# Optimization experiments

Measured on AMD Instinct MI355X. Metric: run time of the kernel, lower is better.

Reference implementation:

```python
import jax, jax.numpy as jnp
import numpy as np

PARENTS = np.array([-1, 0, 1, 1, 1])
NECK_CHAIN = np.array([1, 0])  # neck joint (1) up to root (0)
B, V, F, J, S, E = 512, 5023, 9976, 5, 100, 50
L_STAT, L_DYN, L_FULL, N_BUCKET = 51, 17, 68, 79


def rodrigues(rvec):
    """Axis-angle [N,3] -> rotation matrices [N,3,3]."""
    angle = jnp.linalg.norm(rvec + 1e-8, axis=-1, keepdims=True)  # [N,1]
    axis = rvec / angle
    s = jnp.sin(angle)[..., None]
    c = jnp.cos(angle)[..., None]
    rx, ry, rz = axis[:, 0], axis[:, 1], axis[:, 2]
    z = jnp.zeros_like(rx)
    K = jnp.stack([z, -rz, ry, rz, z, -rx, -ry, rx, z], axis=-1).reshape(-1, 3, 3)
    I = jnp.eye(3, dtype=rvec.dtype)
    return I + s * K + (1.0 - c) * (K @ K)


def verts2lmk(vertices, faces, lmk_faces_idx, lmk_bary):
    lmk_faces = faces[lmk_faces_idx]                               # [B,L,3]
    lmk_verts = jax.vmap(lambda v, f: v[f])(vertices, lmk_faces)   # [B,L,3verts,3xyz]
    return jnp.einsum('blfc,blf->blc', lmk_verts, lmk_bary)


def setup_inputs() -> dict:
    key = jax.random.key(0)
    ks = jax.random.split(key, 16)
    shape_params = jax.random.normal(ks[0], (B, S), jnp.float32)
    expression_params = jax.random.normal(ks[1], (B, E), jnp.float32)
    pose_params = 0.2 * jax.random.normal(ks[2], (B, 6), jnp.float32)
    eye_pose_params = 0.1 * jax.random.normal(ks[3], (B, 6), jnp.float32)
    v_template = jax.random.normal(ks[4], (V, 3), jnp.float32) * 0.1
    shapedirs = jax.random.normal(ks[5], (V, 3, S + E), jnp.float32) * 0.01
    posedirs = jax.random.normal(ks[6], ((J - 1) * 9, V * 3), jnp.float32) * 0.01
    jr = jax.random.uniform(ks[7], (J, V), jnp.float32)
    J_regressor = jr / jnp.sum(jr, axis=1, keepdims=True)
    lbs_weights = jax.nn.softmax(jax.random.normal(ks[8], (V, J), jnp.float32), axis=-1)
    faces = jax.random.randint(ks[9], (F, 3), 0, V)
    lmk_faces_idx = jax.random.randint(ks[10], (L_STAT,), 0, F)
    lb = jax.random.uniform(ks[11], (L_STAT, 3), jnp.float32) + 1e-3
    lmk_bary_coords = lb / jnp.sum(lb, axis=-1, keepdims=True)
    dynamic_lmk_faces_idx = jax.random.randint(ks[12], (N_BUCKET, L_DYN), 0, F)
    db = jax.random.uniform(ks[13], (N_BUCKET, L_DYN, 3), jnp.float32) + 1e-3
    dynamic_lmk_bary_coords = db / jnp.sum(db, axis=-1, keepdims=True)
    full_lmk_faces_idx = jax.random.randint(ks[14], (L_FULL,), 0, F)
    fb = jax.random.uniform(ks[15], (L_FULL, 3), jnp.float32) + 1e-3
    full_lmk_bary_coords = fb / jnp.sum(fb, axis=-1, keepdims=True)
    return {
        'shape_params': shape_params, 'expression_params': expression_params,
        'pose_params': pose_params, 'eye_pose_params': eye_pose_params,
        'v_template': v_template, 'shapedirs': shapedirs, 'posedirs': posedirs,
        'J_regressor': J_regressor, 'lbs_weights': lbs_weights, 'faces': faces,
        'lmk_faces_idx': lmk_faces_idx, 'lmk_bary_coords': lmk_bary_coords,
        'dynamic_lmk_faces_idx': dynamic_lmk_faces_idx,
        'dynamic_lmk_bary_coords': dynamic_lmk_bary_coords,
        'full_lmk_faces_idx': full_lmk_faces_idx,
        'full_lmk_bary_coords': full_lmk_bary_coords,
    }


def reference(shape_params, expression_params, pose_params, eye_pose_params,
              v_template, shapedirs, posedirs, J_regressor, lbs_weights, faces,
              lmk_faces_idx, lmk_bary_coords, dynamic_lmk_faces_idx,
              dynamic_lmk_bary_coords, full_lmk_faces_idx, full_lmk_bary_coords):
    b = shape_params.shape[0]
    nv = v_template.shape[0]
    dt = shape_params.dtype
    betas = jnp.concatenate([shape_params, expression_params], axis=1)          # [B,150]
    neck = jnp.zeros((b, 3), dtype=dt)
    full_pose = jnp.concatenate(
        [pose_params[:, :3], neck, pose_params[:, 3:], eye_pose_params], axis=1)  # [B,15]
    # shape + expression blendshapes
    v_shaped = v_template[None] + jnp.einsum('bl,vcl->bvc', betas, shapedirs)   # [B,V,3]
    joints = jnp.einsum('jv,bvc->bjc', J_regressor, v_shaped)                   # [B,5,3]
    rot_mats = rodrigues(full_pose.reshape(-1, 3)).reshape(b, J, 3, 3)          # [B,5,3,3]
    I3 = jnp.eye(3, dtype=dt)
    pose_feature = (rot_mats[:, 1:] - I3).reshape(b, -1)                        # [B,36]
    v_posed = v_shaped + (pose_feature @ posedirs).reshape(b, nv, 3)
    # kinematic chain -> global joint transforms
    rel_J = joints.at[:, 1:].add(-joints[:, PARENTS[1:]])
    tm = jnp.zeros((b, J, 4, 4), dtype=dt)
    tm = tm.at[:, :, :3, :3].set(rot_mats).at[:, :, :3, 3].set(rel_J).at[:, :, 3, 3].set(1.0)
    chain = [tm[:, 0]]
    for i in range(1, J):
        chain.append(chain[PARENTS[i]] @ tm[:, i])
    A = jnp.stack(chain, axis=1)                                                # [B,5,4,4]
    Rj = jnp.einsum('bjmn,bjn->bjm', A[:, :, :3, :3], joints)
    A_rel = A.at[:, :, :3, 3].add(-Rj)
    # per-vertex skinning
    T = jnp.einsum('vj,bjmn->bvmn', lbs_weights, A_rel)                         # [B,V,4,4]
    vertices = jnp.einsum('bvmn,bvn->bvm', T[:, :, :3, :3], v_posed) + T[:, :, :3, 3]
    # dynamic contour landmark selection from neck kin-chain relative rotation
    aa = full_pose.reshape(b, J, 3)[:, NECK_CHAIN]                              # [B,2,3]
    rc = rodrigues(aa.reshape(-1, 3)).reshape(b, len(NECK_CHAIN), 3, 3)
    rel_rot = jnp.broadcast_to(I3, (b, 3, 3))
    for idx in range(len(NECK_CHAIN)):
        rel_rot = rc[:, idx] @ rel_rot
    sy = jnp.sqrt(rel_rot[:, 0, 0] ** 2 + rel_rot[:, 1, 0] ** 2)
    y_deg = jnp.arctan2(-rel_rot[:, 2, 0], sy) * (180.0 / np.pi)
    y_rot = jnp.round(jnp.minimum(y_deg, 39.0)).astype(jnp.int32)
    neg_mask = y_rot < 0
    big_neg = y_rot < -39
    neg_vals = jnp.where(big_neg, 78, 39 - y_rot)
    y_rot = jnp.where(neg_mask, neg_vals, y_rot)                                # [B] in [0,79)
    dyn_faces = dynamic_lmk_faces_idx[y_rot]                                    # [B,17]
    dyn_bary = dynamic_lmk_bary_coords[y_rot]                                   # [B,17,3]
    lf = jnp.concatenate([dyn_faces, jnp.broadcast_to(lmk_faces_idx[None], (b, lmk_faces_idx.shape[0]))], axis=1)
    lb = jnp.concatenate([dyn_bary, jnp.broadcast_to(lmk_bary_coords[None], (b,) + lmk_bary_coords.shape)], axis=1)
    landmarks2d = verts2lmk(vertices, faces, lf, lb)
    ff = jnp.broadcast_to(full_lmk_faces_idx[None], (b, full_lmk_faces_idx.shape[0]))
    fb = jnp.broadcast_to(full_lmk_bary_coords[None], (b,) + full_lmk_bary_coords.shape)
    landmarks3d = verts2lmk(vertices, faces, ff, fb)
    return (vertices, landmarks2d, landmarks3d)
```

## Files before the change

### kernel.cpp

```cpp
#include <hip/hip_runtime.h>
#include <cstddef>
#include <cstdint>

#define cB   512
#define cV   5023
#define cS   100
#define cE   50
#define cJ   5
#define cLD  17
#define cLF  68

#define cV3    15069
#define cNPAD  15072
#define cKPAD  192

#define OUT_V  ((size_t)cB * cV * 3)
#define OUT_L  ((size_t)cB * cLF * 3)

#define WS_BTN   ((size_t)0)
#define WS_ATM   (WS_BTN + (size_t)cNPAD * 96)
#define WS_JS    (WS_ATM + (size_t)cB * 96)
#define WS_AREL  (WS_JS + 2272)
#define WS_PF    (WS_AREL + (size_t)cB * 60)
#define WS_YROT  (WS_PF + (size_t)cB * 36)

typedef __attribute__((ext_vector_type(8))) short short8;
typedef __attribute__((ext_vector_type(4))) float f32x4;

__device__ __forceinline__ unsigned short f2bf(float x) {
  unsigned int u = __float_as_uint(x);
  u = (u + 0x7fffu + ((u >> 16) & 1u)) >> 16;
  return (unsigned short)u;
}

__device__ __forceinline__ void rodrigues9(float rx, float ry, float rz, float* R) {
  float a0 = rx + 1e-8f, a1 = ry + 1e-8f, a2 = rz + 1e-8f;
  float angle = sqrtf(a0 * a0 + a1 * a1 + a2 * a2);
  float inv = 1.0f / angle;
  float x = rx * inv, y = ry * inv, z = rz * inv;
  float s = sinf(angle), c = cosf(angle);
  float t = 1.0f - c;
  float xy = x * y, xz = x * z, yz = y * z;
  R[0] = 1.0f - t * (y * y + z * z);
  R[1] = -s * z + t * xy;
  R[2] =  s * y + t * xz;
  R[3] =  s * z + t * xy;
  R[4] = 1.0f - t * (x * x + z * z);
  R[5] = -s * x + t * yz;
  R[6] = -s * y + t * xz;
  R[7] =  s * x + t * yz;
  R[8] = 1.0f - t * (x * x + y * y);
}

__global__ void k_js(const float* __restrict__ jreg, const float* __restrict__ sd,
                     const float* __restrict__ vt, float* __restrict__ JS) {
  int t = threadIdx.x;
  if (t >= 453) return;
  int c = t / 151, l = t - c * 151;
  int v0 = blockIdx.x * 40;
  int v1 = v0 + 40; if (v1 > cV) v1 = cV;
  float acc[5] = {0.f, 0.f, 0.f, 0.f, 0.f};
  for (int v = v0; v < v1; ++v) {
    float x = (l < 150) ? sd[(size_t)(v * 3 + c) * 150 + l] : vt[v * 3 + c];
#pragma unroll
    for (int j = 0; j < 5; ++j)
      acc[j] = fmaf(jreg[j * cV + v], x, acc[j]);
  }
#pragma unroll
  for (int j = 0; j < 5; ++j)
    atomicAdd(&JS[(j * 3 + c) * 151 + l], acc[j]);
}

__global__ void k_batch(const float* __restrict__ shp, const float* __restrict__ expr,
                        const float* __restrict__ pose, const float* __restrict__ eyep,
                        const float* __restrict__ JSg, float* __restrict__ Arel,
                        float* __restrict__ pf, int* __restrict__ yrot) {
  __shared__ float js[2272];
  for (int i = threadIdx.x; i < 2265; i += 64) js[i] = JSg[i];
  __syncthreads();
  int b = blockIdx.x * 64 + threadIdx.x;
  if (b >= cB) return;
  float jnt[5][3];
#pragma unroll
  for (int j = 0; j < 5; ++j)
#pragma unroll
    for (int c = 0; c < 3; ++c)
      jnt[j][c] = js[(j * 3 + c) * 151 + 150];
  for (int l = 0; l < 150; ++l) {
    float beta = (l < cS) ? shp[b * cS + l] : expr[b * cE + (l - cS)];
#pragma unroll
    for (int j = 0; j < 5; ++j)
#pragma unroll
      for (int c = 0; c < 3; ++c)
        jnt[j][c] = fmaf(beta, js[(j * 3 + c) * 151 + l], jnt[j][c]);
  }
  float fp[5][3];
  fp[0][0] = pose[b * 6 + 0]; fp[0][1] = pose[b * 6 + 1]; fp[0][2] = pose[b * 6 + 2];
  fp[1][0] = 0.f; fp[1][1] = 0.f; fp[1][2] = 0.f;
  fp[2][0] = pose[b * 6 + 3]; fp[2][1] = pose[b * 6 + 4]; fp[2][2] = pose[b * 6 + 5];
  fp[3][0] = eyep[b * 6 + 0]; fp[3][1] = eyep[b * 6 + 1]; fp[3][2] = eyep[b * 6 + 2];
  fp[4][0] = eyep[b * 6 + 3]; fp[4][1] = eyep[b * 6 + 4]; fp[4][2] = eyep[b * 6 + 5];
  float R[5][9];
#pragma unroll
  for (int j = 0; j < 5; ++j) rodrigues9(fp[j][0], fp[j][1], fp[j][2], R[j]);
#pragma unroll
  for (int j = 1; j < 5; ++j)
#pragma unroll
    for (int r = 0; r < 9; ++r) {
      float id = (r == 0 || r == 4 || r == 8) ? 1.f : 0.f;
      pf[b * 36 + (j - 1) * 9 + r] = R[j][r] - id;
    }
  float rel[5][3];
#pragma unroll
  for (int c = 0; c < 3; ++c) {
    rel[0][c] = jnt[0][c];
    rel[1][c] = jnt[1][c] - jnt[0][c];
    rel[2][c] = jnt[2][c] - jnt[1][c];
    rel[3][c] = jnt[3][c] - jnt[1][c];
    rel[4][c] = jnt[4][c] - jnt[1][c];
  }
  float GR[5][9], Gt[5][3];
#pragma unroll
  for (int r = 0; r < 9; ++r) GR[0][r] = R[0][r];
#pragma unroll
  for (int c = 0; c < 3; ++c) Gt[0][c] = rel[0][c];
  const int par[5] = {0, 0, 1, 1, 1};
#pragma unroll
  for (int j = 1; j < 5; ++j) {
    int p = par[j];
#pragma unroll
    for (int r = 0; r < 3; ++r) {
#pragma unroll
      for (int cc = 0; cc < 3; ++cc)
        GR[j][r * 3 + cc] = GR[p][r * 3 + 0] * R[j][0 + cc] +
                            GR[p][r * 3 + 1] * R[j][3 + cc] +
                            GR[p][r * 3 + 2] * R[j][6 + cc];
      Gt[j][r] = Gt[p][r] + GR[p][r * 3 + 0] * rel[j][0] +
                            GR[p][r * 3 + 1] * rel[j][1] +
                            GR[p][r * 3 + 2] * rel[j][2];
    }
  }
#pragma unroll
  for (int j = 0; j < 5; ++j)
#pragma unroll
    for (int r = 0; r < 3; ++r) {
      float tj = Gt[j][r] - (GR[j][r * 3 + 0] * jnt[j][0] +
                             GR[j][r * 3 + 1] * jnt[j][1] +
                             GR[j][r * 3 + 2] * jnt[j][2]);
      Arel[b * 60 + j * 12 + r * 4 + 0] = GR[j][r * 3 + 0];
      Arel[b * 60 + j * 12 + r * 4 + 1] = GR[j][r * 3 + 1];
      Arel[b * 60 + j * 12 + r * 4 + 2] = GR[j][r * 3 + 2];
      Arel[b * 60 + j * 12 + r * 4 + 3] = tj;
    }
  float Ra[9], Rb[9];
  rodrigues9(fp[1][0], fp[1][1], fp[1][2], Ra);
  rodrigues9(fp[0][0], fp[0][1], fp[0][2], Rb);
  float r00 = Rb[0] * Ra[0] + Rb[1] * Ra[3] + Rb[2] * Ra[6];
  float r10 = Rb[3] * Ra[0] + Rb[4] * Ra[3] + Rb[5] * Ra[6];
  float r20 = Rb[6] * Ra[0] + Rb[7] * Ra[3] + Rb[8] * Ra[6];
  float sy = sqrtf(r00 * r00 + r10 * r10);
  float ydeg = atan2f(-r20, sy) * 57.29577951308232f;
  int y = (int)rintf(fminf(ydeg, 39.0f));
  if (y < 0) y = (y < -39) ? 78 : (39 - y);
  yrot[b] = y;
}

#define QB ((size_t)cNPAD * 48)
__global__ void k_prep(const float* __restrict__ sd, const float* __restrict__ shp,
                       const float* __restrict__ expr, const float* __restrict__ pfm,
                       unsigned int* __restrict__ btn_u2, unsigned int* __restrict__ atm_u2) {
  size_t idx = (size_t)blockIdx.x * 256 + threadIdx.x;
  unsigned short o[4];
  if (idx < QB) {
    int n = (int)(idx / 48), kq = (int)(idx - (size_t)n * 48);
#pragma unroll
    for (int j = 0; j < 4; ++j) {
      int k = kq * 4 + j;
      float v = (n < cV3 && k < 150) ? sd[(size_t)n * 150 + k] : 0.f;
      o[j] = f2bf(v);
    }
    btn_u2[idx * 2 + 0] = (unsigned int)o[0] | ((unsigned int)o[1] << 16);
    btn_u2[idx * 2 + 1] = (unsigned int)o[2] | ((unsigned int)o[3] << 16);
  } else {
    size_t r = idx - QB;
    int m = (int)(r / 48), kq = (int)(r - (size_t)m * 48);
#pragma unroll
    for (int j = 0; j < 4; ++j) {
      int k = kq * 4 + j;
      float v;
      if (k < cS)            v = shp[m * cS + k];
      else if (k < 150)      v = expr[m * cE + (k - cS)];
      else if (k < 186)      v = pfm[m * 36 + (k - 150)];
      else                   v = 0.f;
      o[j] = f2bf(v);
    }
    atm_u2[r * 2 + 0] = (unsigned int)o[0] | ((unsigned int)o[1] << 16);
    atm_u2[r * 2 + 1] = (unsigned int)o[2] | ((unsigned int)o[3] << 16);
  }
}

__global__ void k_pdT(const float* __restrict__ pd, unsigned int* __restrict__ btn_u) {
  __shared__ unsigned short T[64 * 36];
  const int t = threadIdx.x;
  const int n0 = blockIdx.x * 64;
#pragma unroll
  for (int it = 0; it < 9; ++it) {
    int e = t + it * 256;
    int kk = e >> 6, ln = e & 63;
    int n = n0 + ln;
    float v = (n < cV3) ? pd[(size_t)kk * cV3 + n] : 0.f;
    T[ln * 36 + kk] = f2bf(v);
  }
  __syncthreads();
  for (int e = t; e < 64 * 18; e += 256) {
    int ln = e / 18, d = e - ln * 18;
    int n = n0 + ln;
    if (n < cV3) {
      unsigned int w = (unsigned int)T[ln * 36 + 2 * d] |
                       ((unsigned int)T[ln * 36 + 2 * d + 1] << 16);
      btn_u[(size_t)n * 96 + 75 + d] = w;
    }
  }
}

__global__ __launch_bounds__(256) void k_main(
    const unsigned short* __restrict__ BTn, const unsigned short* __restrict__ ATm,
    const float* __restrict__ Arel, const float* __restrict__ vtempl,
    const float* __restrict__ lbw, float* __restrict__ out) {
  __shared__ __align__(16) unsigned short smem[32000];
  unsigned short* As = smem;
  unsigned short* Bs = smem + 12800;
  float* Pf  = (float*)smem;
  float* ArL = ((float*)smem) + 6528;

  const int t  = threadIdx.x;
  const int nb = blockIdx.x, mb = blockIdx.y;

  {
    const unsigned short* bsrc = BTn + (size_t)nb * 96 * 192;
    const unsigned short* asrc = ATm + (size_t)mb * 64 * 192;
#pragma unroll
    for (int it = 0; it < 15; ++it) {
      int e = t + it * 256;
      uint4 val;
      int row, col;
      if (e < 2304) {
        row = e / 24; col = e - row * 24;
        val = *(const uint4*)(bsrc + (size_t)e * 8);
        *(uint4*)(Bs + row * 200 + col * 8) = val;
      } else {
        int e2 = e - 2304;
        row = e2 / 24; col = e2 - row * 24;
        val = *(const uint4*)(asrc + (size_t)e2 * 8);
        *(uint4*)(As + row * 200 + col * 8) = val;
      }
    }
  }
  __syncthreads();

  const int w = t >> 6, L = t & 63;
  const int wm = w >> 1, wn = w & 1;
  const int lr = L & 15, lq = L >> 4;

  f32x4 acc[2][3];
#pragma unroll
  for (int mt = 0; mt < 2; ++mt)
#pragma unroll
    for (int nt = 0; nt < 3; ++nt) acc[mt][nt] = (f32x4){0.f, 0.f, 0.f, 0.f};

#pragma unroll
  for (int ks = 0; ks < 6; ++ks) {
    const int ko = ks * 32 + lq * 8;
    short8 af[2], bf[3];
#pragma unroll
    for (int mt = 0; mt < 2; ++mt)
      af[mt] = *(const short8*)(As + (wm * 32 + mt * 16 + lr) * 200 + ko);
#pragma unroll
    for (int nt = 0; nt < 3; ++nt)
      bf[nt] = *(const short8*)(Bs + (wn * 48 + nt * 16 + lr) * 200 + ko);
#pragma unroll
    for (int mt = 0; mt < 2; ++mt)
#pragma unroll
      for (int nt = 0; nt < 3; ++nt)
        acc[mt][nt] = __builtin_amdgcn_mfma_f32_16x16x32_bf16(af[mt], bf[nt], acc[mt][nt], 0, 0, 0);
  }
  __syncthreads();

#pragma unroll
  for (int mt = 0; mt < 2; ++mt)
#pragma unroll
    for (int nt = 0; nt < 3; ++nt) {
      int m_base = wm * 32 + mt * 16 + lq * 4;
      int n_loc  = wn * 48 + nt * 16 + lr;
      *(f32x4*)(Pf + n_loc * 68 + m_base) = acc[mt][nt];
    }
  for (int e = t; e < 3840; e += 256)
    ArL[e] = Arel[(size_t)mb * 64 * 60 + e];
  __syncthreads();

  const int v_loc = t & 31, bgrp = t >> 5;
  const int v = nb * 32 + v_loc;
  float wj[5], vtl[3];
  const bool vok = (v < cV);
#pragma unroll
  for (int j = 0; j < 5; ++j) wj[j] = vok ? lbw[v * 5 + j] : 0.f;
#pragma unroll
  for (int c = 0; c < 3; ++c) vtl[c] = vok ? vtempl[v * 3 + c] : 0.f;

#pragma unroll
  for (int i = 0; i < 8; ++i) {
    const int b_loc = bgrp * 8 + i;
    const float* q = ArL + b_loc * 60;
    float px = Pf[(v_loc * 3 + 0) * 68 + b_loc] + vtl[0];
    float py = Pf[(v_loc * 3 + 1) * 68 + b_loc] + vtl[1];
    float pz = Pf[(v_loc * 3 + 2) * 68 + b_loc] + vtl[2];
    float o0 = 0.f, o1 = 0.f, o2 = 0.f;
#pragma unroll
    for (int j = 0; j < 5; ++j) {
      f32x4 q0 = *(const f32x4*)(q + j * 12);
      f32x4 q1 = *(const f32x4*)(q + j * 12 + 4);
      f32x4 q2 = *(const f32x4*)(q + j * 12 + 8);
      float s0 = q0.x * px + q0.y * py + q0.z * pz + q0.w;
      float s1 = q1.x * px + q1.y * py + q1.z * pz + q1.w;
      float s2 = q2.x * px + q2.y * py + q2.z * pz + q2.w;
      o0 = fmaf(wj[j], s0, o0);
      o1 = fmaf(wj[j], s1, o1);
      o2 = fmaf(wj[j], s2, o2);
    }
    if (vok) {
      const int b = mb * 64 + b_loc;
      size_t off = ((size_t)b * cV + v) * 3;
      out[off + 0] = o0;
      out[off + 1] = o1;
      out[off + 2] = o2;
    }
  }
}

__global__ void k_lmk(const float* __restrict__ verts, const int* __restrict__ faces,
                      const int* __restrict__ lmkf, const float* __restrict__ lmkb,
                      const int* __restrict__ dynf, const float* __restrict__ dynb,
                      const int* __restrict__ fullf, const float* __restrict__ fullb,
                      const int* __restrict__ yrot, float* __restrict__ out) {
  int id = blockIdx.x * 256 + threadIdx.x;
  if (id >= cB * cLF) return;
  int b = id / cLF, l = id - b * cLF;
  const float* vb = verts + (size_t)b * cV * 3;
  {
    int f; float w0, w1, w2;
    if (l < cLD) {
      int yb = yrot[b];
      f = dynf[yb * cLD + l];
      const float* bp = dynb + ((size_t)yb * cLD + l) * 3;
      w0 = bp[0]; w1 = bp[1]; w2 = bp[2];
    } else {
      f = lmkf[l - cLD];
      const float* bp = lmkb + (size_t)(l - cLD) * 3;
      w0 = bp[0]; w1 = bp[1]; w2 = bp[2];
    }
    int i0 = faces[f * 3 + 0] * 3, i1 = faces[f * 3 + 1] * 3, i2 = faces[f * 3 + 2] * 3;
    size_t o = OUT_V + ((size_t)b * cLF + l) * 3;
    out[o + 0] = w0 * vb[i0 + 0] + w1 * vb[i1 + 0] + w2 * vb[i2 + 0];
    out[o + 1] = w0 * vb[i0 + 1] + w1 * vb[i1 + 1] + w2 * vb[i2 + 1];
    out[o + 2] = w0 * vb[i0 + 2] + w1 * vb[i1 + 2] + w2 * vb[i2 + 2];
  }
  {
    int f = fullf[l];
    const float* bp = fullb + (size_t)l * 3;
    float w0 = bp[0], w1 = bp[1], w2 = bp[2];
    int i0 = faces[f * 3 + 0] * 3, i1 = faces[f * 3 + 1] * 3, i2 = faces[f * 3 + 2] * 3;
    size_t o = OUT_V + OUT_L + ((size_t)b * cLF + l) * 3;
    out[o + 0] = w0 * vb[i0 + 0] + w1 * vb[i1 + 0] + w2 * vb[i2 + 0];
    out[o + 1] = w0 * vb[i0 + 1] + w1 * vb[i1 + 1] + w2 * vb[i2 + 1];
    out[o + 2] = w0 * vb[i0 + 2] + w1 * vb[i1 + 2] + w2 * vb[i2 + 2];
  }
}

extern "C" void kernel_launch(void* const* d_in, const int* in_sizes, int n_in,
                              void* d_out, int out_size, void* d_ws, size_t ws_size,
                              hipStream_t stream) {
  (void)in_sizes; (void)n_in; (void)out_size; (void)ws_size;
  const float* shp  = (const float*)d_in[0];
  const float* expr = (const float*)d_in[1];
  const float* pose = (const float*)d_in[2];
  const float* eyep = (const float*)d_in[3];
  const float* vt   = (const float*)d_in[4];
  const float* sd   = (const float*)d_in[5];
  const float* pd   = (const float*)d_in[6];
  const float* jreg = (const float*)d_in[7];
  const float* lbw  = (const float*)d_in[8];
  const int*   fcs  = (const int*)d_in[9];
  const int*   lmkf = (const int*)d_in[10];
  const float* lmkb = (const float*)d_in[11];
  const int*   dynf = (const int*)d_in[12];
  const float* dynb = (const float*)d_in[13];
  const int*   fullf= (const int*)d_in[14];
  const float* fullb= (const float*)d_in[15];
  float* out = (float*)d_out;
  float* ws  = (float*)d_ws;

  unsigned short* BTn = (unsigned short*)(ws + WS_BTN);
  unsigned short* ATm = (unsigned short*)(ws + WS_ATM);
  float* JS   = ws + WS_JS;
  float* Arel = ws + WS_AREL;
  float* pf   = ws + WS_PF;
  int*   yrot = (int*)(ws + WS_YROT);

  hipMemsetAsync(JS, 0, 2272 * sizeof(float), stream);
  k_js<<<126, 512, 0, stream>>>(jreg, sd, vt, JS);
  k_batch<<<8, 64, 0, stream>>>(shp, expr, pose, eyep, JS, Arel, pf, yrot);
  k_prep<<<2922, 256, 0, stream>>>(sd, shp, expr, pf,
                                   (unsigned int*)BTn, (unsigned int*)ATm);
  k_pdT<<<236, 256, 0, stream>>>(pd, (unsigned int*)BTn);
  k_main<<<dim3(157, 8), 256, 0, stream>>>(BTn, ATm, Arel, vt, lbw, out);
  k_lmk<<<136, 256, 0, stream>>>(out, fcs, lmkf, lmkb, dynf, dynb, fullf, fullb, yrot, out);
}
```

Baseline: 200.6 us.

## Shrink main-kernel LDS, hold A fragments in registers, and retune helper kernels

The main GEMM kernel now loads its A operand fragments straight from global memory into registers and stages only the B tile in LDS. It reads Arel directly from global instead of copying it to shared memory, which cuts LDS use and adds an occupancy hint of 4 blocks. The batch kernel gains 256 threads that cooperatively stage shape/expression coefficients into LDS, the landmark kernel splits its two landmark sets across separate threads, and the joint-regression kernel uses smaller vertex chunks with more blocks and unrolling. The cost is higher register pressure from holding 12 A fragments per thread, and uncoalesced global reads of A and Arel.

```diff
diff --git a/kernel.cpp b/kernel.cpp
--- a/kernel.cpp
+++ b/kernel.cpp
@@ -57,9 +57,10 @@
   int t = threadIdx.x;
   if (t >= 453) return;
   int c = t / 151, l = t - c * 151;
-  int v0 = blockIdx.x * 40;
-  int v1 = v0 + 40; if (v1 > cV) v1 = cV;
+  int v0 = blockIdx.x * 32;
+  int v1 = v0 + 32; if (v1 > cV) v1 = cV;
   float acc[5] = {0.f, 0.f, 0.f, 0.f, 0.f};
+#pragma unroll 8
   for (int v = v0; v < v1; ++v) {
     float x = (l < 150) ? sd[(size_t)(v * 3 + c) * 150 + l] : vt[v * 3 + c];
 #pragma unroll
@@ -71,15 +72,27 @@
     atomicAdd(&JS[(j * 3 + c) * 151 + l], acc[j]);
 }
 
-__global__ void k_batch(const float* __restrict__ shp, const float* __restrict__ expr,
-                        const float* __restrict__ pose, const float* __restrict__ eyep,
-                        const float* __restrict__ JSg, float* __restrict__ Arel,
-                        float* __restrict__ pf, int* __restrict__ yrot) {
+__global__ __launch_bounds__(256) void k_batch(
+    const float* __restrict__ shp, const float* __restrict__ expr,
+    const float* __restrict__ pose, const float* __restrict__ eyep,
+    const float* __restrict__ JSg, float* __restrict__ Arel,
+    float* __restrict__ pf, int* __restrict__ yrot) {
   __shared__ float js[2272];
-  for (int i = threadIdx.x; i < 2265; i += 64) js[i] = JSg[i];
+  __shared__ float sb[64 * 153];
+  const int t = threadIdx.x;
+  const int b0 = blockIdx.x * 64;
+  for (int i = t; i < 2265; i += 256) js[i] = JSg[i];
+  for (int e = t; e < 6400; e += 256) {
+    int bl = e / 100, l = e - bl * 100;
+    sb[bl * 153 + l] = shp[(size_t)(b0 + bl) * 100 + l];
+  }
+  for (int e = t; e < 3200; e += 256) {
+    int bl = e / 50, l = e - bl * 50;
+    sb[bl * 153 + 100 + l] = expr[(size_t)(b0 + bl) * 50 + l];
+  }
   __syncthreads();
-  int b = blockIdx.x * 64 + threadIdx.x;
-  if (b >= cB) return;
+  if (t >= 64) return;
+  int b = b0 + t;
   float jnt[5][3];
 #pragma unroll
   for (int j = 0; j < 5; ++j)
@@ -87,7 +100,7 @@
     for (int c = 0; c < 3; ++c)
       jnt[j][c] = js[(j * 3 + c) * 151 + 150];
   for (int l = 0; l < 150; ++l) {
-    float beta = (l < cS) ? shp[b * cS + l] : expr[b * cE + (l - cS)];
+    float beta = sb[t * 153 + l];
 #pragma unroll
     for (int j = 0; j < 5; ++j)
 #pragma unroll
@@ -223,45 +236,41 @@
   }
 }
 
-__global__ __launch_bounds__(256) void k_main(
+__global__ __launch_bounds__(256, 4) void k_main(
     const unsigned short* __restrict__ BTn, const unsigned short* __restrict__ ATm,
     const float* __restrict__ Arel, const float* __restrict__ vtempl,
     const float* __restrict__ lbw, float* __restrict__ out) {
-  __shared__ __align__(16) unsigned short smem[32000];
-  unsigned short* As = smem;
-  unsigned short* Bs = smem + 12800;
-  float* Pf  = (float*)smem;
-  float* ArL = ((float*)smem) + 6528;
+  __shared__ __align__(16) unsigned short smem[19200];
+  float* Pf = (float*)smem;
 
   const int t  = threadIdx.x;
   const int nb = blockIdx.x, mb = blockIdx.y;
-
-  {
-    const unsigned short* bsrc = BTn + (size_t)nb * 96 * 192;
-    const unsigned short* asrc = ATm + (size_t)mb * 64 * 192;
-#pragma unroll
-    for (int it = 0; it < 15; ++it) {
-      int e = t + it * 256;
-      uint4 val;
-      int row, col;
-      if (e < 2304) {
-        row = e / 24; col = e - row * 24;
-        val = *(const uint4*)(bsrc + (size_t)e * 8);
-        *(uint4*)(Bs + row * 200 + col * 8) = val;
-      } else {
-        int e2 = e - 2304;
-        row = e2 / 24; col = e2 - row * 24;
-        val = *(const uint4*)(asrc + (size_t)e2 * 8);
-        *(uint4*)(As + row * 200 + col * 8) = val;
-      }
-    }
-  }
-  __syncthreads();
-
   const int w = t >> 6, L = t & 63;
   const int wm = w >> 1, wn = w & 1;
   const int lr = L & 15, lq = L >> 4;
 
+  const unsigned short* bsrc = BTn + (size_t)nb * 96 * 192;
+  uint4 bst[9];
+#pragma unroll
+  for (int it = 0; it < 9; ++it)
+    bst[it] = *(const uint4*)(bsrc + ((size_t)(t + it * 256)) * 8);
+
+  const unsigned short* abase = ATm + ((size_t)mb * 64 + wm * 32 + lr) * 192 + lq * 8;
+  short8 af[6][2];
+#pragma unroll
+  for (int ks = 0; ks < 6; ++ks)
+#pragma unroll
+    for (int mt = 0; mt < 2; ++mt)
+      af[ks][mt] = *(const short8*)(abase + (size_t)mt * 16 * 192 + ks * 32);
+
+#pragma unroll
+  for (int it = 0; it < 9; ++it) {
+    int e = t + it * 256;
+    int row = e / 24, col = e - row * 24;
+    *(uint4*)(smem + row * 200 + col * 8) = bst[it];
+  }
+  __syncthreads();
+
   f32x4 acc[2][3];
 #pragma unroll
   for (int mt = 0; mt < 2; ++mt)
@@ -271,18 +280,15 @@
 #pragma unroll
   for (int ks = 0; ks < 6; ++ks) {
     const int ko = ks * 32 + lq * 8;
-    short8 af[2], bf[3];
+    short8 bf[3];
+#pragma unroll
+    for (int nt = 0; nt < 3; ++nt)
+      bf[nt] = *(const short8*)(smem + (wn * 48 + nt * 16 + lr) * 200 + ko);
 #pragma unroll
     for (int mt = 0; mt < 2; ++mt)
-      af[mt] = *(const short8*)(As + (wm * 32 + mt * 16 + lr) * 200 + ko);
-#pragma unroll
-    for (int nt = 0; nt < 3; ++nt)
-      bf[nt] = *(const short8*)(Bs + (wn * 48 + nt * 16 + lr) * 200 + ko);
-#pragma unroll
-    for (int mt = 0; mt < 2; ++mt)
 #pragma unroll
       for (int nt = 0; nt < 3; ++nt)
-        acc[mt][nt] = __builtin_amdgcn_mfma_f32_16x16x32_bf16(af[mt], bf[nt], acc[mt][nt], 0, 0, 0);
+        acc[mt][nt] = __builtin_amdgcn_mfma_f32_16x16x32_bf16(af[ks][mt], bf[nt], acc[mt][nt], 0, 0, 0);
   }
   __syncthreads();
 
@@ -294,8 +300,6 @@
       int n_loc  = wn * 48 + nt * 16 + lr;
       *(f32x4*)(Pf + n_loc * 68 + m_base) = acc[mt][nt];
     }
-  for (int e = t; e < 3840; e += 256)
-    ArL[e] = Arel[(size_t)mb * 64 * 60 + e];
   __syncthreads();
 
   const int v_loc = t & 31, bgrp = t >> 5;
@@ -310,7 +314,7 @@
 #pragma unroll
   for (int i = 0; i < 8; ++i) {
     const int b_loc = bgrp * 8 + i;
-    const float* q = ArL + b_loc * 60;
+    const float* q = Arel + ((size_t)mb * 64 + b_loc) * 60;
     float px = Pf[(v_loc * 3 + 0) * 68 + b_loc] + vtl[0];
     float py = Pf[(v_loc * 3 + 1) * 68 + b_loc] + vtl[1];
     float pz = Pf[(v_loc * 3 + 2) * 68 + b_loc] + vtl[2];
@@ -343,11 +347,13 @@
                       const int* __restrict__ fullf, const float* __restrict__ fullb,
                       const int* __restrict__ yrot, float* __restrict__ out) {
   int id = blockIdx.x * 256 + threadIdx.x;
-  if (id >= cB * cLF) return;
-  int b = id / cLF, l = id - b * cLF;
+  if (id >= cB * cLF * 2) return;
+  int sel = id & 1;
+  int r = id >> 1;
+  int b = r / cLF, l = r - b * cLF;
   const float* vb = verts + (size_t)b * cV * 3;
-  {
-    int f; float w0, w1, w2;
+  int f; float w0, w1, w2; size_t o;
+  if (sel == 0) {
     if (l < cLD) {
       int yb = yrot[b];
       f = dynf[yb * cLD + l];
@@ -358,22 +364,17 @@
       const float* bp = lmkb + (size_t)(l - cLD) * 3;
       w0 = bp[0]; w1 = bp[1]; w2 = bp[2];
     }
-    int i0 = faces[f * 3 + 0] * 3, i1 = faces[f * 3 + 1] * 3, i2 = faces[f * 3 + 2] * 3;
-    size_t o = OUT_V + ((size_t)b * cLF + l) * 3;
-    out[o + 0] = w0 * vb[i0 + 0] + w1 * vb[i1 + 0] + w2 * vb[i2 + 0];
-    out[o + 1] = w0 * vb[i0 + 1] + w1 * vb[i1 + 1] + w2 * vb[i2 + 1];
-    out[o + 2] = w0 * vb[i0 + 2] + w1 * vb[i1 + 2] + w2 * vb[i2 + 2];
-  }
-  {
-    int f = fullf[l];
+    o = OUT_V + ((size_t)b * cLF + l) * 3;
+  } else {
+    f = fullf[l];
     const float* bp = fullb + (size_t)l * 3;
-    float w0 = bp[0], w1 = bp[1], w2 = bp[2];
-    int i0 = faces[f * 3 + 0] * 3, i1 = faces[f * 3 + 1] * 3, i2 = faces[f * 3 + 2] * 3;
-    size_t o = OUT_V + OUT_L + ((size_t)b * cLF + l) * 3;
-    out[o + 0] = w0 * vb[i0 + 0] + w1 * vb[i1 + 0] + w2 * vb[i2 + 0];
-    out[o + 1] = w0 * vb[i0 + 1] + w1 * vb[i1 + 1] + w2 * vb[i2 + 1];
-    out[o + 2] = w0 * vb[i0 + 2] + w1 * vb[i1 + 2] + w2 * vb[i2 + 2];
-  }
+    w0 = bp[0]; w1 = bp[1]; w2 = bp[2];
+    o = OUT_V + OUT_L + ((size_t)b * cLF + l) * 3;
+  }
+  int i0 = faces[f * 3 + 0] * 3, i1 = faces[f * 3 + 1] * 3, i2 = faces[f * 3 + 2] * 3;
+  out[o + 0] = w0 * vb[i0 + 0] + w1 * vb[i1 + 0] + w2 * vb[i2 + 0];
+  out[o + 1] = w0 * vb[i0 + 1] + w1 * vb[i1 + 1] + w2 * vb[i2 + 1];
+  out[o + 2] = w0 * vb[i0 + 2] + w1 * vb[i1 + 2] + w2 * vb[i2 + 2];
 }
 
 extern "C" void kernel_launch(void* const* d_in, const int* in_sizes, int n_in,
@@ -407,11 +408,11 @@
   int*   yrot = (int*)(ws + WS_YROT);
 
   hipMemsetAsync(JS, 0, 2272 * sizeof(float), stream);
-  k_js<<<126, 512, 0, stream>>>(jreg, sd, vt, JS);
-  k_batch<<<8, 64, 0, stream>>>(shp, expr, pose, eyep, JS, Arel, pf, yrot);
+  k_js<<<157, 512, 0, stream>>>(jreg, sd, vt, JS);
+  k_batch<<<8, 256, 0, stream>>>(shp, expr, pose, eyep, JS, Arel, pf, yrot);
   k_prep<<<2922, 256, 0, stream>>>(sd, shp, expr, pf,
                                    (unsigned int*)BTn, (unsigned int*)ATm);
   k_pdT<<<236, 256, 0, stream>>>(pd, (unsigned int*)BTn);
   k_main<<<dim3(157, 8), 256, 0, stream>>>(BTn, ATm, Arel, vt, lbw, out);
-  k_lmk<<<136, 256, 0, stream>>>(out, fcs, lmkf, lmkb, dynf, dynb, fullf, fullb, yrot, out);
-}
+  k_lmk<<<272, 256, 0, stream>>>(out, fcs, lmkf, lmkb, dynf, dynb, fullf, fullb, yrot, out);
+}
```

Result: slower. 210.4 us (+4.9%).
